# Kernel tuning notes

Measured on AMD Instinct MI355X. Metric: run time of the kernel, lower is better.

## Reference

```python
import jax, jax.numpy as jnp
import numpy as np

EMBED_DIM = 512
NUM_HEADS = 8
HEAD_DIM = EMBED_DIM // NUM_HEADS


def setup_inputs() -> dict:
    key = jax.random.key(0)
    ks = jax.random.split(key, 6)
    B, S, D = 2, 4096, EMBED_DIM
    scale = 1.0 / np.sqrt(D)
    inputs = jax.random.normal(ks[0], (B, S, D), dtype=jnp.float32)
    Wq = jax.random.normal(ks[1], (D, D), dtype=jnp.float32) * scale
    Wk = jax.random.normal(ks[2], (D, D), dtype=jnp.float32) * scale
    Wv = jax.random.normal(ks[3], (D, D), dtype=jnp.float32) * scale
    Wo = jax.random.normal(ks[4], (D, D), dtype=jnp.float32) * scale
    zeros = jnp.zeros((D,), dtype=jnp.float32)
    return {"inputs": inputs, "Wq": Wq, "bq": zeros, "Wk": Wk, "bk": zeros,
            "Wv": Wv, "bv": zeros, "Wo": Wo, "bo": zeros}


def _split_heads(x, B, S):
    # [B,S,D] -> [B,H,S,hd]
    return x.reshape(B, S, NUM_HEADS, HEAD_DIM).transpose(0, 2, 1, 3)


def reference(inputs, Wq, bq, Wk, bk, Wv, bv, Wo, bo):
    B, S, D = inputs.shape
    q = _split_heads(inputs @ Wq + bq, B, S)
    k = _split_heads(inputs @ Wk + bk, B, S)
    v = _split_heads(inputs @ Wv + bv, B, S)
    scale = 1.0 / jnp.sqrt(jnp.asarray(HEAD_DIM, dtype=inputs.dtype))
    # full [B,H,S,S] score matrix, as in the original naive SDPA
    scores = jnp.einsum('bhqd,bhkd->bhqk', q, k) * scale
    weights = jax.nn.softmax(scores, axis=-1)
    attn = jnp.einsum('bhqk,bhkd->bhqd', weights, v)
    attn = attn.transpose(0, 2, 1, 3).reshape(B, S, D)
    return attn @ Wo + bo
```

## Files before the change

### kernel.cpp

```cpp
#include <hip/hip_runtime.h>
#include <hip/hip_bf16.h>
#include <stdint.h>


typedef __bf16 bf16x8 __attribute__((ext_vector_type(8)));
typedef float f32x4 __attribute__((ext_vector_type(4)));

using as1_void = __attribute__((address_space(1))) void;
using as3_void = __attribute__((address_space(3))) void;

__device__ __forceinline__ void gload16(const void* g, void* l) {
    __builtin_amdgcn_global_load_lds((const as1_void*)g, (as3_void*)l, 16, 0, 0);
}

__device__ __forceinline__ f32x4 mfma16(bf16x8 a, bf16x8 b, f32x4 c) {
    return __builtin_amdgcn_mfma_f32_16x16x32_bf16(a, b, c, 0, 0, 0);
}

__device__ __forceinline__ uint32_t pkbf(float a, float b) {
    union { __hip_bfloat16 h[2]; uint32_t u; } r;
    r.h[0] = __float2bfloat16(a);
    r.h[1] = __float2bfloat16(b);
    return r.u;
}

__global__ void cvt_x(const float* __restrict__ in, __hip_bfloat16* __restrict__ out, int n) {
    int i = (blockIdx.x * 256 + threadIdx.x) * 4;
    if (i >= n) return;
    float4 v = *reinterpret_cast<const float4*>(in + i);
    union { __hip_bfloat16 h[4]; uint2 u; } r;
    r.h[0] = __float2bfloat16(v.x);
    r.h[1] = __float2bfloat16(v.y);
    r.h[2] = __float2bfloat16(v.z);
    r.h[3] = __float2bfloat16(v.w);
    *reinterpret_cast<uint2*>(out + i) = r.u;
}

__global__ void cvt_wt(const float* __restrict__ w0, const float* __restrict__ w1,
                       const float* __restrict__ w2, const float* __restrict__ w3,
                       __hip_bfloat16* __restrict__ o0, __hip_bfloat16* __restrict__ o1,
                       __hip_bfloat16* __restrict__ o2, __hip_bfloat16* __restrict__ o3) {
    const float* W; __hip_bfloat16* O;
    switch (blockIdx.z) {
        case 0: W = w0; O = o0; break;
        case 1: W = w1; O = o1; break;
        case 2: W = w2; O = o2; break;
        default: W = w3; O = o3; break;
    }
    __shared__ float t[32][33];
    int n0 = blockIdx.x * 32, k0 = blockIdx.y * 32;
    int tx = threadIdx.x, ty = threadIdx.y;
    for (int j = 0; j < 4; ++j)
        t[ty + 8 * j][tx] = W[(size_t)(k0 + ty + 8 * j) * 512 + n0 + tx];
    __syncthreads();
    for (int j = 0; j < 4; ++j)
        O[(size_t)(n0 + ty + 8 * j) * 512 + k0 + tx] = __float2bfloat16(t[tx][ty + 8 * j]);
}

__global__ __launch_bounds__(256, 2) void gemm_qkv(
    const __hip_bfloat16* __restrict__ A, const __hip_bfloat16* __restrict__ Bt,
    const float* __restrict__ bq, const float* __restrict__ bk, const float* __restrict__ bv,
    __hip_bfloat16* __restrict__ Qb, __hip_bfloat16* __restrict__ Kb,
    __hip_bfloat16* __restrict__ Vtb, float qs)
{
    const int K = 512;
    __shared__ __hip_bfloat16 Abuf[128 * 32];
    __shared__ __hip_bfloat16 Bbuf[128 * 32];
    const int tid = threadIdx.x, w = tid >> 6, lane = tid & 63;
    const int col = lane & 15, quad = lane >> 4;
    const int wr = w >> 1, wc = w & 1;
    const int tileN = blockIdx.x * 128, tileM = blockIdx.y * 128;

    f32x4 acc[4][4] = {};

    for (int k0 = 0; k0 < K; k0 += 32) {
        for (int i = 0; i < 2; ++i) {
            int g = w * 2 + i;
            int chunk = g * 64 + lane;
            int row = chunk >> 2, c8 = chunk & 3;
            gload16(A + (size_t)(tileM + row) * K + k0 + c8 * 8, Abuf + g * 512);
            gload16(Bt + (size_t)(tileN + row) * K + k0 + c8 * 8, Bbuf + g * 512);
        }
        __syncthreads();
        bf16x8 af[4], bfr[4];
        for (int mt = 0; mt < 4; ++mt)
            af[mt] = *reinterpret_cast<const bf16x8*>(Abuf + (wr * 64 + mt * 16 + col) * 32 + quad * 8);
        for (int nt = 0; nt < 4; ++nt)
            bfr[nt] = *reinterpret_cast<const bf16x8*>(Bbuf + (wc * 64 + nt * 16 + col) * 32 + quad * 8);
        for (int mt = 0; mt < 4; ++mt)
            for (int nt = 0; nt < 4; ++nt)
                acc[mt][nt] = mfma16(af[mt], bfr[nt], acc[mt][nt]);
        __syncthreads();
    }

    const int seg = (tileN + wc * 64) >> 9;
    const float* bias = (seg == 0) ? bq : (seg == 1) ? bk : bv;
    const float scale = (seg == 0) ? qs : 1.0f;
    __hip_bfloat16* outp = (seg == 0) ? Qb : (seg == 1) ? Kb : Vtb;

    for (int mt = 0; mt < 4; ++mt) {
        for (int nt = 0; nt < 4; ++nt) {
            int n = tileN + wc * 64 + nt * 16 + col;
            int nn = n & 511, h = nn >> 6, d = nn & 63;
            float bn = bias[nn];
            for (int r = 0; r < 4; ++r) {
                int m = tileM + wr * 64 + mt * 16 + quad * 4 + r;
                int b = m >> 12, s = m & 4095;
                float v = (acc[mt][nt][r] + bn) * scale;
                size_t off;
                if (seg < 2) off = (((size_t)(b * 8 + h) * 4096 + s) << 6) + d;
                else         off = (((size_t)(b * 8 + h) * 64 + d) << 12) + s;
                outp[off] = __float2bfloat16(v);
            }
        }
    }
}

__global__ __launch_bounds__(256, 2) void gemm_out(
    const __hip_bfloat16* __restrict__ A, const __hip_bfloat16* __restrict__ Bt,
    const float* __restrict__ bias, float* __restrict__ out)
{
    const int N = 512, K = 512;
    __shared__ __hip_bfloat16 Abuf[128 * 32];
    __shared__ __hip_bfloat16 Bbuf[128 * 32];
    const int tid = threadIdx.x, w = tid >> 6, lane = tid & 63;
    const int col = lane & 15, quad = lane >> 4;
    const int wr = w >> 1, wc = w & 1;
    const int tileN = blockIdx.x * 128, tileM = blockIdx.y * 128;

    f32x4 acc[4][4] = {};

    for (int k0 = 0; k0 < K; k0 += 32) {
        for (int i = 0; i < 2; ++i) {
            int g = w * 2 + i;
            int chunk = g * 64 + lane;
            int row = chunk >> 2, c8 = chunk & 3;
            gload16(A + (size_t)(tileM + row) * K + k0 + c8 * 8, Abuf + g * 512);
            gload16(Bt + (size_t)(tileN + row) * K + k0 + c8 * 8, Bbuf + g * 512);
        }
        __syncthreads();
        bf16x8 af[4], bfr[4];
        for (int mt = 0; mt < 4; ++mt)
            af[mt] = *reinterpret_cast<const bf16x8*>(Abuf + (wr * 64 + mt * 16 + col) * 32 + quad * 8);
        for (int nt = 0; nt < 4; ++nt)
            bfr[nt] = *reinterpret_cast<const bf16x8*>(Bbuf + (wc * 64 + nt * 16 + col) * 32 + quad * 8);
        for (int mt = 0; mt < 4; ++mt)
            for (int nt = 0; nt < 4; ++nt)
                acc[mt][nt] = mfma16(af[mt], bfr[nt], acc[mt][nt]);
        __syncthreads();
    }

    for (int mt = 0; mt < 4; ++mt) {
        for (int nt = 0; nt < 4; ++nt) {
            int n = tileN + wc * 64 + nt * 16 + col;
            float bn = bias[n];
            for (int r = 0; r < 4; ++r) {
                int m = tileM + wr * 64 + mt * 16 + quad * 4 + r;
                out[(size_t)m * N + n] = acc[mt][nt][r] + bn;
            }
        }
    }
}

__global__ __launch_bounds__(256) void flash(
    const __hip_bfloat16* __restrict__ Q,
    const __hip_bfloat16* __restrict__ Kq,
    const __hip_bfloat16* __restrict__ Vt,
    __hip_bfloat16* __restrict__ attnb)
{
    __shared__ __hip_bfloat16 KT[2][4096];
    __shared__ __hip_bfloat16 VB[2][4096];
    __shared__ uint32_t TB[4][1024];

    const int bh = blockIdx.y, b = bh >> 3, h = bh & 7;
    const int tid = threadIdx.x, w = tid >> 6, lane = tid & 63;
    const int col = lane & 15, quad = lane >> 4;
    const int q0 = blockIdx.x * 128 + w * 32;
    const int c7 = col & 7;

    const __hip_bfloat16* Qh = Q + (size_t)bh * 4096 * 64;
    const __hip_bfloat16* Kh = Kq + (size_t)bh * 4096 * 64;
    const __hip_bfloat16* Vh = Vt + (size_t)bh * 64 * 4096;

    bf16x8 aq[2][2];
    for (int qh = 0; qh < 2; ++qh)
        for (int ks = 0; ks < 2; ++ks)
            aq[qh][ks] = *reinterpret_cast<const bf16x8*>(
                Qh + (size_t)(q0 + qh * 16 + col) * 64 + ks * 32 + quad * 8);

    const __hip_bfloat16* ksrc[2];
    const __hip_bfloat16* vsrc[2];
    int ldsoff[2];
    for (int i = 0; i < 2; ++i) {
        int c = i * 256 + tid;
        int row = c >> 3, s8 = (c & 7) ^ (row & 7);
        ksrc[i] = Kh + row * 64 + s8 * 8;
        vsrc[i] = Vh + (size_t)row * 4096 + s8 * 8;
        ldsoff[i] = (i * 256 + w * 64) * 8;
    }

    bf16x8 ones;
    for (int j = 0; j < 8; ++j) ones[j] = (__bf16)1.0f;

    f32x4 o[4][2] = {};
    f32x4 accl[2] = {};
    f32x4 sc[2][4][2];

    uint32_t* TBw = &TB[w][0];
    uint2* TBw2 = reinterpret_cast<uint2*>(TBw);

    gload16(ksrc[0], &KT[0][ldsoff[0]]);
    gload16(ksrc[1], &KT[0][ldsoff[1]]);
    gload16(vsrc[0], &VB[0][ldsoff[0]]);
    gload16(vsrc[1], &VB[0][ldsoff[1]]);
    gload16(ksrc[0] + 4096, &KT[1][ldsoff[0]]);
    gload16(ksrc[1] + 4096, &KT[1][ldsoff[1]]);
    __syncthreads();

    for (int kg = 0; kg < 4; ++kg)
        for (int qh = 0; qh < 2; ++qh)
            sc[0][kg][qh] = (f32x4){0.f, 0.f, 0.f, 0.f};
    for (int ks = 0; ks < 2; ++ks)
        for (int kg = 0; kg < 4; ++kg) {
            bf16x8 ak = *reinterpret_cast<const bf16x8*>(
                &KT[0][(kg * 16 + col) * 64 + (((ks * 4 + quad) ^ c7) << 3)]);
            for (int qh = 0; qh < 2; ++qh)
                sc[0][kg][qh] = mfma16(ak, aq[qh][ks], sc[0][kg][qh]);
        }
    __syncthreads();

#define FLASH_BODY(KT_, P_)                                                     \
    {                                                                           \
        const int kt_ = (KT_);                                                  \
        int kk = kt_ + 2; if (kk > 63) kk = 63;     \
        gload16(ksrc[0] + (size_t)kk * 4096, &KT[(P_)][ldsoff[0]]);             \
        gload16(ksrc[1] + (size_t)kk * 4096, &KT[(P_)][ldsoff[1]]);             \
        gload16(vsrc[0] + (size_t)(kt_ + 1) * 64, &VB[1 - (P_)][ldsoff[0]]);    \
        gload16(vsrc[1] + (size_t)(kt_ + 1) * 64, &VB[1 - (P_)][ldsoff[1]]);    \
                           \
        for (int kg = 0; kg < 4; ++kg)                                          \
            for (int qh = 0; qh < 2; ++qh) {                                    \
                f32x4 v = sc[(P_)][kg][qh];                                     \
                uint2 u;                                                        \
                u.x = pkbf(__builtin_amdgcn_exp2f(v[0]),                        \
                           __builtin_amdgcn_exp2f(v[1]));                       \
                u.y = pkbf(__builtin_amdgcn_exp2f(v[2]),                        \
                           __builtin_amdgcn_exp2f(v[3]));                       \
                TBw2[(qh * 16 + col) * 16 +                                     \
                     (((kg * 2 + (quad >> 1)) ^ c7) << 1) + (quad & 1)] = u;    \
            }                                                                   \
              \
        for (int kg = 0; kg < 4; ++kg)                                          \
            for (int qh = 0; qh < 2; ++qh)                                      \
                sc[1 - (P_)][kg][qh] = (f32x4){0.f, 0.f, 0.f, 0.f};             \
        for (int ks = 0; ks < 2; ++ks)                                          \
            for (int kg = 0; kg < 4; ++kg) {                                    \
                bf16x8 ak = *reinterpret_cast<const bf16x8*>(                   \
                    &KT[1 - (P_)][(kg * 16 + col) * 64 +                        \
                                  (((ks * 4 + quad) ^ c7) << 3)]);              \
                for (int qh = 0; qh < 2; ++qh)                                  \
                    sc[1 - (P_)][kg][qh] =                                      \
                        mfma16(ak, aq[qh][ks], sc[1 - (P_)][kg][qh]);           \
            }                                                                   \
                                                    \
        bf16x8 bp[2][2];                                                        \
        for (int qh = 0; qh < 2; ++qh)                                          \
            for (int ks = 0; ks < 2; ++ks)                                      \
                bp[qh][ks] = *reinterpret_cast<const bf16x8*>(                  \
                    &TBw[(qh * 16 + col) * 32 + (((ks * 4 + quad) ^ c7) << 2)]);\
        for (int ks = 0; ks < 2; ++ks) {                                        \
            for (int dt = 0; dt < 4; ++dt) {                                    \
                bf16x8 av = *reinterpret_cast<const bf16x8*>(                   \
                    &VB[(P_)][(dt * 16 + col) * 64 +                            \
                              (((ks * 4 + quad) ^ c7) << 3)]);                  \
                for (int qh = 0; qh < 2; ++qh)                                  \
                    o[dt][qh] = mfma16(av, bp[qh][ks], o[dt][qh]);              \
            }                                                                   \
            accl[0] = mfma16(ones, bp[0][ks], accl[0]);                         \
            accl[1] = mfma16(ones, bp[1][ks], accl[1]);                         \
        }                                                                       \
        __syncthreads();                                                        \
    }

    FLASH_BODY(0, 0)
    for (int kth = 0; kth < 31; ++kth) {
        FLASH_BODY(2 * kth + 1, 1)
        FLASH_BODY(2 * kth + 2, 0)
    }
    {
        for (int kg = 0; kg < 4; ++kg)
            for (int qh = 0; qh < 2; ++qh) {
                f32x4 v = sc[1][kg][qh];
                uint2 u;
                u.x = pkbf(__builtin_amdgcn_exp2f(v[0]), __builtin_amdgcn_exp2f(v[1]));
                u.y = pkbf(__builtin_amdgcn_exp2f(v[2]), __builtin_amdgcn_exp2f(v[3]));
                TBw2[(qh * 16 + col) * 16 + (((kg * 2 + (quad >> 1)) ^ c7) << 1) + (quad & 1)] = u;
            }
        bf16x8 bp[2][2];
        for (int qh = 0; qh < 2; ++qh)
            for (int ks = 0; ks < 2; ++ks)
                bp[qh][ks] = *reinterpret_cast<const bf16x8*>(
                    &TBw[(qh * 16 + col) * 32 + (((ks * 4 + quad) ^ c7) << 2)]);
        for (int ks = 0; ks < 2; ++ks) {
            for (int dt = 0; dt < 4; ++dt) {
                bf16x8 av = *reinterpret_cast<const bf16x8*>(
                    &VB[1][(dt * 16 + col) * 64 + (((ks * 4 + quad) ^ c7) << 3)]);
                for (int qh = 0; qh < 2; ++qh)
                    o[dt][qh] = mfma16(av, bp[qh][ks], o[dt][qh]);
            }
            accl[0] = mfma16(ones, bp[0][ks], accl[0]);
            accl[1] = mfma16(ones, bp[1][ks], accl[1]);
        }
    }
#undef FLASH_BODY

    for (int qh = 0; qh < 2; ++qh) {
        float inv = 1.0f / accl[qh][0];
        int s = q0 + qh * 16 + col;
        __hip_bfloat16* dst = attnb + ((size_t)b * 4096 + s) * 512 + h * 64 + quad * 4;
        for (int dt = 0; dt < 4; ++dt) {
            union { __hip_bfloat16 hh[4]; ushort4 v4; } pk;
            for (int r = 0; r < 4; ++r)
                pk.hh[r] = __float2bfloat16(o[dt][qh][r] * inv);
            *reinterpret_cast<ushort4*>(dst + dt * 16) = pk.v4;
        }
    }
}

extern "C" void kernel_launch(void* const* d_in, const int* in_sizes, int n_in,
                              void* d_out, int out_size, void* d_ws, size_t ws_size,
                              hipStream_t stream) {
    const float* X  = (const float*)d_in[0];
    const float* Wq = (const float*)d_in[1];
    const float* bq = (const float*)d_in[2];
    const float* Wk = (const float*)d_in[3];
    const float* bk = (const float*)d_in[4];
    const float* Wv = (const float*)d_in[5];
    const float* bv = (const float*)d_in[6];
    const float* Wo = (const float*)d_in[7];
    const float* bo = (const float*)d_in[8];
    float* out = (float*)d_out;

    char* ws = (char*)d_ws;
    __hip_bfloat16* Xb  = (__hip_bfloat16*)(ws);
    __hip_bfloat16* Wqt = (__hip_bfloat16*)(ws + ((size_t)8 << 20));
    __hip_bfloat16* Wkt = Wqt + 512 * 512;
    __hip_bfloat16* Wvt = Wkt + 512 * 512;
    __hip_bfloat16* Wot = Wvt + 512 * 512;
    __hip_bfloat16* Qb  = (__hip_bfloat16*)(ws + ((size_t)10 << 20));
    __hip_bfloat16* Kb  = (__hip_bfloat16*)(ws + ((size_t)18 << 20));
    __hip_bfloat16* Vtb = (__hip_bfloat16*)(ws + ((size_t)26 << 20));
    __hip_bfloat16* Atb = (__hip_bfloat16*)(ws + ((size_t)34 << 20));

    const int M = 8192, K = 512;

    cvt_x<<<4096, 256, 0, stream>>>(X, Xb, M * K);
    cvt_wt<<<dim3(16, 16, 4), dim3(32, 8), 0, stream>>>(Wq, Wk, Wv, Wo, Wqt, Wkt, Wvt, Wot);

    const float qs = 0.125f * 1.4426950408889634f;
    gemm_qkv<<<dim3(12, 64), 256, 0, stream>>>(Xb, Wqt, bq, bk, bv, Qb, Kb, Vtb, qs);

    flash<<<dim3(32, 16), 256, 0, stream>>>(Qb, Kb, Vtb, Atb);

    gemm_out<<<dim3(4, 64), 256, 0, stream>>>(Atb, Wot, bo, out);
}
```

Baseline: 217.3 us.

## Fuse fp32-to-bf16 conversion and weight transpose into GEMM tile loads

```diff
diff --git a/kernel.cpp b/kernel.cpp
--- a/kernel.cpp
+++ b/kernel.cpp
@@ -24,84 +24,81 @@
     return r.u;
 }
 
-__global__ void cvt_x(const float* __restrict__ in, __hip_bfloat16* __restrict__ out, int n) {
-    int i = (blockIdx.x * 256 + threadIdx.x) * 4;
-    if (i >= n) return;
-    float4 v = *reinterpret_cast<const float4*>(in + i);
-    union { __hip_bfloat16 h[4]; uint2 u; } r;
-    r.h[0] = __float2bfloat16(v.x);
-    r.h[1] = __float2bfloat16(v.y);
-    r.h[2] = __float2bfloat16(v.z);
-    r.h[3] = __float2bfloat16(v.w);
-    *reinterpret_cast<uint2*>(out + i) = r.u;
-}
-
-__global__ void cvt_wt(const float* __restrict__ w0, const float* __restrict__ w1,
-                       const float* __restrict__ w2, const float* __restrict__ w3,
-                       __hip_bfloat16* __restrict__ o0, __hip_bfloat16* __restrict__ o1,
-                       __hip_bfloat16* __restrict__ o2, __hip_bfloat16* __restrict__ o3) {
-    const float* W; __hip_bfloat16* O;
-    switch (blockIdx.z) {
-        case 0: W = w0; O = o0; break;
-        case 1: W = w1; O = o1; break;
-        case 2: W = w2; O = o2; break;
-        default: W = w3; O = o3; break;
-    }
-    __shared__ float t[32][33];
-    int n0 = blockIdx.x * 32, k0 = blockIdx.y * 32;
-    int tx = threadIdx.x, ty = threadIdx.y;
-    for (int j = 0; j < 4; ++j)
-        t[ty + 8 * j][tx] = W[(size_t)(k0 + ty + 8 * j) * 512 + n0 + tx];
-    __syncthreads();
-    for (int j = 0; j < 4; ++j)
-        O[(size_t)(n0 + ty + 8 * j) * 512 + k0 + tx] = __float2bfloat16(t[tx][ty + 8 * j]);
-}
-
-__global__ __launch_bounds__(256, 2) void gemm_qkv(
-    const __hip_bfloat16* __restrict__ A, const __hip_bfloat16* __restrict__ Bt,
+__global__ __launch_bounds__(256, 3) void gemm_qkv(
+    const float* __restrict__ X,
+    const float* __restrict__ Wq, const float* __restrict__ Wk, const float* __restrict__ Wv,
     const float* __restrict__ bq, const float* __restrict__ bk, const float* __restrict__ bv,
     __hip_bfloat16* __restrict__ Qb, __hip_bfloat16* __restrict__ Kb,
     __hip_bfloat16* __restrict__ Vtb, float qs)
 {
-    const int K = 512;
     __shared__ __hip_bfloat16 Abuf[128 * 32];
     __shared__ __hip_bfloat16 Bbuf[128 * 32];
     const int tid = threadIdx.x, w = tid >> 6, lane = tid & 63;
     const int col = lane & 15, quad = lane >> 4;
     const int wr = w >> 1, wc = w & 1;
     const int tileN = blockIdx.x * 128, tileM = blockIdx.y * 128;
+    const int seg = blockIdx.x >> 2;
+    const int nb0 = tileN & 511;
+    const float* W = (seg == 0) ? Wq : (seg == 1) ? Wk : Wv;
+
+    const int arow = tid >> 1, ah = (tid & 1) * 16;
+    const int kp = tid >> 4, part = tid & 15;
+    const int bgrp = (((kp >> 2) ^ (part & 3)) << 2) + (kp & 3);
+    uint32_t* B32 = reinterpret_cast<uint32_t*>(Bbuf);
 
     f32x4 acc[4][4] = {};
 
-    for (int k0 = 0; k0 < K; k0 += 32) {
-        for (int i = 0; i < 2; ++i) {
-            int g = w * 2 + i;
-            int chunk = g * 64 + lane;
-            int row = chunk >> 2, c8 = chunk & 3;
-            gload16(A + (size_t)(tileM + row) * K + k0 + c8 * 8, Abuf + g * 512);
-            gload16(Bt + (size_t)(tileN + row) * K + k0 + c8 * 8, Bbuf + g * 512);
-        }
+    for (int k0 = 0; k0 < 512; k0 += 32) {
+        const float* ap = X + (size_t)(tileM + arow) * 512 + k0 + ah;
+        float4 a0 = *reinterpret_cast<const float4*>(ap);
+        float4 a1 = *reinterpret_cast<const float4*>(ap + 4);
+        float4 a2 = *reinterpret_cast<const float4*>(ap + 8);
+        float4 a3 = *reinterpret_cast<const float4*>(ap + 12);
+        union { uint32_t u[4]; int4 v; } pa0, pa1;
+        pa0.u[0] = pkbf(a0.x, a0.y); pa0.u[1] = pkbf(a0.z, a0.w);
+        pa0.u[2] = pkbf(a1.x, a1.y); pa0.u[3] = pkbf(a1.z, a1.w);
+        pa1.u[0] = pkbf(a2.x, a2.y); pa1.u[1] = pkbf(a2.z, a2.w);
+        pa1.u[2] = pkbf(a3.x, a3.y); pa1.u[3] = pkbf(a3.z, a3.w);
+        const float* bp0 = W + (size_t)(k0 + 2 * kp) * 512 + nb0 + part * 8;
+        float4 b00 = *reinterpret_cast<const float4*>(bp0);
+        float4 b01 = *reinterpret_cast<const float4*>(bp0 + 4);
+        float4 b10 = *reinterpret_cast<const float4*>(bp0 + 512);
+        float4 b11 = *reinterpret_cast<const float4*>(bp0 + 516);
+        *reinterpret_cast<int4*>(Abuf + arow * 32 + ah) = pa0.v;
+        *reinterpret_cast<int4*>(Abuf + arow * 32 + ah + 8) = pa1.v;
+        B32[(part * 8 + 0) * 16 + bgrp] = pkbf(b00.x, b10.x);
+        B32[(part * 8 + 1) * 16 + bgrp] = pkbf(b00.y, b10.y);
+        B32[(part * 8 + 2) * 16 + bgrp] = pkbf(b00.z, b10.z);
+        B32[(part * 8 + 3) * 16 + bgrp] = pkbf(b00.w, b10.w);
+        B32[(part * 8 + 4) * 16 + bgrp] = pkbf(b01.x, b11.x);
+        B32[(part * 8 + 5) * 16 + bgrp] = pkbf(b01.y, b11.y);
+        B32[(part * 8 + 6) * 16 + bgrp] = pkbf(b01.z, b11.z);
+        B32[(part * 8 + 7) * 16 + bgrp] = pkbf(b01.w, b11.w);
         __syncthreads();
+
         bf16x8 af[4], bfr[4];
         for (int mt = 0; mt < 4; ++mt)
-            af[mt] = *reinterpret_cast<const bf16x8*>(Abuf + (wr * 64 + mt * 16 + col) * 32 + quad * 8);
-        for (int nt = 0; nt < 4; ++nt)
-            bfr[nt] = *reinterpret_cast<const bf16x8*>(Bbuf + (wc * 64 + nt * 16 + col) * 32 + quad * 8);
+            af[mt] = *reinterpret_cast<const bf16x8*>(
+                Abuf + (wr * 64 + mt * 16 + col) * 32 + quad * 8);
+        for (int nt = 0; nt < 4; ++nt) {
+            int n = wc * 64 + nt * 16 + col;
+            int g = quad ^ ((2 * nt + (col >> 3)) & 3);
+            bfr[nt] = *reinterpret_cast<const bf16x8*>(Bbuf + n * 32 + g * 8);
+        }
         for (int mt = 0; mt < 4; ++mt)
             for (int nt = 0; nt < 4; ++nt)
                 acc[mt][nt] = mfma16(af[mt], bfr[nt], acc[mt][nt]);
         __syncthreads();
     }
 
-    const int seg = (tileN + wc * 64) >> 9;
     const float* bias = (seg == 0) ? bq : (seg == 1) ? bk : bv;
     const float scale = (seg == 0) ? qs : 1.0f;
     __hip_bfloat16* outp = (seg == 0) ? Qb : (seg == 1) ? Kb : Vtb;
 
     for (int mt = 0; mt < 4; ++mt) {
         for (int nt = 0; nt < 4; ++nt) {
-            int n = tileN + wc * 64 + nt * 16 + col;
-            int nn = n & 511, h = nn >> 6, d = nn & 63;
+            int nn = nb0 + wc * 64 + nt * 16 + col;
+            int h = nn >> 6, d = nn & 63;
             float bn = bias[nn];
             for (int r = 0; r < 4; ++r) {
                 int m = tileM + wr * 64 + mt * 16 + quad * 4 + r;
@@ -116,47 +113,66 @@
     }
 }
 
-__global__ __launch_bounds__(256, 2) void gemm_out(
-    const __hip_bfloat16* __restrict__ A, const __hip_bfloat16* __restrict__ Bt,
+__global__ __launch_bounds__(256, 3) void gemm_out(
+    const __hip_bfloat16* __restrict__ A, const float* __restrict__ W,
     const float* __restrict__ bias, float* __restrict__ out)
 {
-    const int N = 512, K = 512;
-    __shared__ __hip_bfloat16 Abuf[128 * 32];
+    __shared__ __hip_bfloat16 Abuf[64 * 32];
     __shared__ __hip_bfloat16 Bbuf[128 * 32];
     const int tid = threadIdx.x, w = tid >> 6, lane = tid & 63;
     const int col = lane & 15, quad = lane >> 4;
     const int wr = w >> 1, wc = w & 1;
-    const int tileN = blockIdx.x * 128, tileM = blockIdx.y * 128;
-
-    f32x4 acc[4][4] = {};
-
-    for (int k0 = 0; k0 < K; k0 += 32) {
-        for (int i = 0; i < 2; ++i) {
-            int g = w * 2 + i;
-            int chunk = g * 64 + lane;
-            int row = chunk >> 2, c8 = chunk & 3;
-            gload16(A + (size_t)(tileM + row) * K + k0 + c8 * 8, Abuf + g * 512);
-            gload16(Bt + (size_t)(tileN + row) * K + k0 + c8 * 8, Bbuf + g * 512);
-        }
+    const int tileN = blockIdx.x * 128, tileM = blockIdx.y * 64;
+
+    const int kp = tid >> 4, part = tid & 15;
+    const int bgrp = (((kp >> 2) ^ (part & 3)) << 2) + (kp & 3);
+    uint32_t* B32 = reinterpret_cast<uint32_t*>(Bbuf);
+
+    f32x4 acc[2][4] = {};
+
+    for (int k0 = 0; k0 < 512; k0 += 32) {
+        {
+            int row = tid >> 2, c8 = tid & 3;
+            gload16(A + (size_t)(tileM + row) * 512 + k0 + c8 * 8,
+                    Abuf + (w * 64 + lane) * 8);
+        }
+        const float* bp0 = W + (size_t)(k0 + 2 * kp) * 512 + tileN + part * 8;
+        float4 b00 = *reinterpret_cast<const float4*>(bp0);
+        float4 b01 = *reinterpret_cast<const float4*>(bp0 + 4);
+        float4 b10 = *reinterpret_cast<const float4*>(bp0 + 512);
+        float4 b11 = *reinterpret_cast<const float4*>(bp0 + 516);
+        B32[(part * 8 + 0) * 16 + bgrp] = pkbf(b00.x, b10.x);
+        B32[(part * 8 + 1) * 16 + bgrp] = pkbf(b00.y, b10.y);
+        B32[(part * 8 + 2) * 16 + bgrp] = pkbf(b00.z, b10.z);
+        B32[(part * 8 + 3) * 16 + bgrp] = pkbf(b00.w, b10.w);
+        B32[(part * 8 + 4) * 16 + bgrp] = pkbf(b01.x, b11.x);
+        B32[(part * 8 + 5) * 16 + bgrp] = pkbf(b01.y, b11.y);
+        B32[(part * 8 + 6) * 16 + bgrp] = pkbf(b01.z, b11.z);
+        B32[(part * 8 + 7) * 16 + bgrp] = pkbf(b01.w, b11.w);
         __syncthreads();
-        bf16x8 af[4], bfr[4];
-        for (int mt = 0; mt < 4; ++mt)
-            af[mt] = *reinterpret_cast<const bf16x8*>(Abuf + (wr * 64 + mt * 16 + col) * 32 + quad * 8);
-        for (int nt = 0; nt < 4; ++nt)
-            bfr[nt] = *reinterpret_cast<const bf16x8*>(Bbuf + (wc * 64 + nt * 16 + col) * 32 + quad * 8);
-        for (int mt = 0; mt < 4; ++mt)
+
+        bf16x8 af[2], bfr[4];
+        for (int mt = 0; mt < 2; ++mt)
+            af[mt] = *reinterpret_cast<const bf16x8*>(
+                Abuf + (wr * 32 + mt * 16 + col) * 32 + quad * 8);
+        for (int nt = 0; nt < 4; ++nt) {
+            int n = wc * 64 + nt * 16 + col;
+            int g = quad ^ ((2 * nt + (col >> 3)) & 3);
+            bfr[nt] = *reinterpret_cast<const bf16x8*>(Bbuf + n * 32 + g * 8);
+        }
+        for (int mt = 0; mt < 2; ++mt)
             for (int nt = 0; nt < 4; ++nt)
                 acc[mt][nt] = mfma16(af[mt], bfr[nt], acc[mt][nt]);
         __syncthreads();
     }
 
-    for (int mt = 0; mt < 4; ++mt) {
+    for (int mt = 0; mt < 2; ++mt) {
         for (int nt = 0; nt < 4; ++nt) {
             int n = tileN + wc * 64 + nt * 16 + col;
             float bn = bias[n];
             for (int r = 0; r < 4; ++r) {
-                int m = tileM + wr * 64 + mt * 16 + quad * 4 + r;
-                out[(size_t)m * N + n] = acc[mt][nt][r] + bn;
+                int m = tileM + wr * 32 + mt * 16 + quad * 4 + r;
+                out[(size_t)m * 512 + n] = acc[mt][nt][r] + bn;
             }
         }
     }
@@ -232,12 +248,11 @@
 #define FLASH_BODY(KT_, P_)                                                     \
     {                                                                           \
         const int kt_ = (KT_);                                                  \
-        int kk = kt_ + 2; if (kk > 63) kk = 63;     \
+        int kk = kt_ + 2; if (kk > 63) kk = 63;                                 \
         gload16(ksrc[0] + (size_t)kk * 4096, &KT[(P_)][ldsoff[0]]);             \
         gload16(ksrc[1] + (size_t)kk * 4096, &KT[(P_)][ldsoff[1]]);             \
         gload16(vsrc[0] + (size_t)(kt_ + 1) * 64, &VB[1 - (P_)][ldsoff[0]]);    \
         gload16(vsrc[1] + (size_t)(kt_ + 1) * 64, &VB[1 - (P_)][ldsoff[1]]);    \
-                           \
         for (int kg = 0; kg < 4; ++kg)                                          \
             for (int qh = 0; qh < 2; ++qh) {                                    \
                 f32x4 v = sc[(P_)][kg][qh];                                     \
@@ -249,7 +264,6 @@
                 TBw2[(qh * 16 + col) * 16 +                                     \
                      (((kg * 2 + (quad >> 1)) ^ c7) << 1) + (quad & 1)] = u;    \
             }                                                                   \
-              \
         for (int kg = 0; kg < 4; ++kg)                                          \
             for (int qh = 0; qh < 2; ++qh)                                      \
                 sc[1 - (P_)][kg][qh] = (f32x4){0.f, 0.f, 0.f, 0.f};             \
@@ -262,7 +276,6 @@
                     sc[1 - (P_)][kg][qh] =                                      \
                         mfma16(ak, aq[qh][ks], sc[1 - (P_)][kg][qh]);           \
             }                                                                   \
-                                                    \
         bf16x8 bp[2][2];                                                        \
         for (int qh = 0; qh < 2; ++qh)                                          \
             for (int ks = 0; ks < 2; ++ks)                                      \
@@ -342,25 +355,14 @@
     float* out = (float*)d_out;
 
     char* ws = (char*)d_ws;
-    __hip_bfloat16* Xb  = (__hip_bfloat16*)(ws);
-    __hip_bfloat16* Wqt = (__hip_bfloat16*)(ws + ((size_t)8 << 20));
-    __hip_bfloat16* Wkt = Wqt + 512 * 512;
-    __hip_bfloat16* Wvt = Wkt + 512 * 512;
-    __hip_bfloat16* Wot = Wvt + 512 * 512;
     __hip_bfloat16* Qb  = (__hip_bfloat16*)(ws + ((size_t)10 << 20));
     __hip_bfloat16* Kb  = (__hip_bfloat16*)(ws + ((size_t)18 << 20));
     __hip_bfloat16* Vtb = (__hip_bfloat16*)(ws + ((size_t)26 << 20));
     __hip_bfloat16* Atb = (__hip_bfloat16*)(ws + ((size_t)34 << 20));
 
-    const int M = 8192, K = 512;
-
-    cvt_x<<<4096, 256, 0, stream>>>(X, Xb, M * K);
-    cvt_wt<<<dim3(16, 16, 4), dim3(32, 8), 0, stream>>>(Wq, Wk, Wv, Wo, Wqt, Wkt, Wvt, Wot);
-
     const float qs = 0.125f * 1.4426950408889634f;
-    gemm_qkv<<<dim3(12, 64), 256, 0, stream>>>(Xb, Wqt, bq, bk, bv, Qb, Kb, Vtb, qs);
-
+
+    gemm_qkv<<<dim3(12, 64), 256, 0, stream>>>(X, Wq, Wk, Wv, bq, bk, bv, Qb, Kb, Vtb, qs);
     flash<<<dim3(32, 16), 256, 0, stream>>>(Qb, Kb, Vtb, Atb);
-
-    gemm_out<<<dim3(4, 64), 256, 0, stream>>>(Atb, Wot, bo, out);
-}
+    gemm_out<<<dim3(4, 128), 256, 0, stream>>>(Atb, Wo, bo, out);
+}
```

Result: slower. 223.0 us (+2.6%).
